# Performance work log

Hardware: AMD Instinct MI355X
Metric: run time of the kernel (lower is better)

## Reference

```python
import jax, jax.numpy as jnp
import numpy as np

N, E = 20000, 320000
FX, FW, FH, H = 256, 128, 128, 4  # x feat, walk feat, hidden=end_embd, heads


def _gat(x, edge_index, W, a_s, a_d, R):
    # W: [H,Fin,Fout]; a_s,a_d: [H,Fout]; R: [Fin,Fout] residual projection
    n = x.shape[0]
    h = jnp.einsum('nf,hfo->hno', x, W)                      # [H,N,Fout]
    src, dst = edge_index[0], edge_index[1]
    s_src = jnp.einsum('hno,ho->nh', h, a_s)                 # [N,H]
    s_dst = jnp.einsum('hno,ho->nh', h, a_d)                 # [N,H]
    e = jax.nn.leaky_relu(s_src[src] + s_dst[dst], 0.2)      # [E,H] per-edge scores
    m = jax.ops.segment_max(e, src, num_segments=n)          # scatter-softmax (stable)
    ex = jnp.exp(e - m[src])
    den = jax.ops.segment_sum(ex, src, num_segments=n)
    alpha = ex / (den[src] + 1e-16)                          # [E,H]
    msg = jnp.transpose(h, (1, 0, 2))[dst] * alpha[:, :, None]        # [E,H,Fout]
    agg = jax.ops.segment_sum(msg, src, num_segments=n).mean(axis=1)  # [N,Fout]
    return jax.nn.elu(agg + x @ R)


def _forward(x, dat, W1, a1s, a1d, R1, W2, a2s, a2d, R2,
             Wd1, ad1s, ad1d, Rd1, Wd2, ad2s, ad2d, Rd2,
             fc1_w, fc1_b, fc2_w, fc2_b, conv_w, conv_b, edge_index):
    x1 = _gat(x, edge_index, W1, a1s, a1d, R1)
    x2 = _gat(x1, edge_index, W2, a2s, a2d, R2)
    d1 = _gat(dat, edge_index, Wd1, ad1s, ad1d, Rd1)
    d2 = _gat(d1, edge_index, Wd2, ad2s, ad2d, Rd2)
    n = x.shape[0]
    # cat on feature dim, transpose, view(1, l*2, end_size, N)
    xd = jnp.concatenate([x1, x2, d1, d2], axis=1).T.reshape(1, 4, FH, n)
    avg = xd.mean(axis=(2, 3))                               # SE global avg pool [1,4]
    att = jax.nn.sigmoid((avg @ fc1_w + fc1_b) @ fc2_w + fc2_b)  # no act between fc1/fc2 (as in source)
    xatt = jax.nn.relu(att[:, :, None, None] * xd)
    y = jnp.einsum('bchn,c->bhn', xatt, conv_w) + conv_b     # 1x1 conv, 4->1 channels
    return y.reshape(FH, n).T                                # dropout = identity (eval)


def setup_inputs():
    key = jax.random.key(0)
    ks = jax.random.split(key, 26)

    def rn(k, shape, s=0.1):
        return jax.random.normal(k, shape, jnp.float32) * s

    return {
        'x': jax.random.normal(ks[0], (N, FX), jnp.float32),
        'dat': jax.random.normal(ks[1], (N, FW), jnp.float32),
        'W1': rn(ks[2], (H, FX, FH)), 'a1s': rn(ks[3], (H, FH)), 'a1d': rn(ks[4], (H, FH)), 'R1': rn(ks[5], (FX, FH)),
        'W2': rn(ks[6], (H, FH, FH)), 'a2s': rn(ks[7], (H, FH)), 'a2d': rn(ks[8], (H, FH)), 'R2': rn(ks[9], (FH, FH)),
        'Wd1': rn(ks[10], (H, FW, FH)), 'ad1s': rn(ks[11], (H, FH)), 'ad1d': rn(ks[12], (H, FH)), 'Rd1': rn(ks[13], (FW, FH)),
        'Wd2': rn(ks[14], (H, FH, FH)), 'ad2s': rn(ks[15], (H, FH)), 'ad2d': rn(ks[16], (H, FH)), 'Rd2': rn(ks[17], (FH, FH)),
        'fc1_w': rn(ks[18], (4, 20)), 'fc1_b': jnp.zeros((20,), jnp.float32),
        'fc2_w': rn(ks[19], (20, 4)), 'fc2_b': jnp.zeros((4,), jnp.float32),
        'conv_w': rn(ks[20], (4,)), 'conv_b': jnp.zeros((), jnp.float32),
        'edge_index': jax.random.randint(ks[21], (2, E), 0, N, dtype=jnp.int32),
    }


def reference(x, dat, W1, a1s, a1d, R1, W2, a2s, a2d, R2,
              Wd1, ad1s, ad1d, Rd1, Wd2, ad2s, ad2d, Rd2,
              fc1_w, fc1_b, fc2_w, fc2_b, conv_w, conv_b, edge_index):
    return _forward(x, dat, W1, a1s, a1d, R1, W2, a2s, a2d, R2,
                    Wd1, ad1s, ad1d, Rd1, Wd2, ad2s, ad2d, Rd2,
                    fc1_w, fc1_b, fc2_w, fc2_b, conv_w, conv_b, edge_index)
```

## Files before the change

### kernel.cpp

```cpp
#include <hip/hip_runtime.h>
#include <hip/hip_bf16.h>
#include <math.h>

#define NN 20000
#define EE 320000
#define FXX 256
#define FWW 128
#define NH 4

typedef __attribute__((ext_vector_type(8))) short short8v;
typedef __attribute__((ext_vector_type(4))) float f32x4;

static __device__ __forceinline__ float bf2f(unsigned short s) {
    unsigned int u = ((unsigned int)s) << 16;
    return __builtin_bit_cast(float, u);
}

static __device__ __forceinline__ unsigned short f2bf_u16(float f) {
    unsigned int u = __builtin_bit_cast(unsigned int, f);
    unsigned int r = 0x7fffu + ((u >> 16) & 1u);
    return (unsigned short)((u + r) >> 16);
}

struct WscItem { const float* W; const float* as_; const float* ad_; int Fin; };
struct WscParams { WscItem t[4]; };

__global__ __launch_bounds__(256) void wsc_kernel(WscParams p, float* __restrict__ wsc)
{
    int L = blockIdx.z;
    WscItem it = p.t[L];
    int wid = threadIdx.x >> 6, lane = threadIdx.x & 63;
    int r = blockIdx.x * 4 + wid;
    if (r >= it.Fin * 4) return;
    int h = r / it.Fin, k = r - h * it.Fin;
    float2 w2 = *(const float2*)(it.W + ((size_t)(h * it.Fin + k)) * 128 + 2 * lane);
    float2 s2 = *(const float2*)(it.as_ + h * 128 + 2 * lane);
    float2 d2 = *(const float2*)(it.ad_ + h * 128 + 2 * lane);
    float vs = w2.x * s2.x + w2.y * s2.y;
    float vd = w2.x * d2.x + w2.y * d2.y;
    #pragma unroll
    for (int o = 32; o; o >>= 1) { vs += __shfl_xor(vs, o); vd += __shfl_xor(vd, o); }
    if (lane == 0) {
        wsc[(size_t)L * 2048 + h * 256 + k] = vs;
        wsc[(size_t)L * 2048 + (4 + h) * 256 + k] = vd;
    }
}

struct WcItem { const float* W; const float* R; __hip_bfloat16* dst; int Fin; int KK; int total; };
struct WcParams { WcItem t[4]; };

__global__ __launch_bounds__(256) void wcomb_kernel(WcParams p)
{
    WcItem it = p.t[blockIdx.z];
    int idx = blockIdx.x * 256 + threadIdx.x;
    if (idx >= it.total) return;
    int c = idx / it.KK;
    int k5 = idx - c * it.KK;
    int f4 = it.Fin * 4;
    float v;
    if (k5 < f4) {
        int h = k5 / it.Fin, k = k5 - h * it.Fin;
        v = 0.25f * it.W[((size_t)(h * it.Fin + k)) * 128 + c];
    } else {
        v = it.R[(size_t)(k5 - f4) * 128 + c];
    }
    it.dst[(size_t)c * it.KK + k5] = __float2bfloat16(v);
}

template<int CF>
__global__ __launch_bounds__(256) void cast_score(const float* __restrict__ Xf,
                                                  __hip_bfloat16* __restrict__ Xb,
                                                  const float* __restrict__ wsc,
                                                  float* __restrict__ ssrc,
                                                  float* __restrict__ sdst)
{
    const int Fin = CF * 64;
    int wid = threadIdx.x >> 6, lane = threadIdx.x & 63;
    int n = blockIdx.x * 4 + wid;
    if (n >= NN) return;
    int c0 = lane * CF;
    float xv[CF];
    #pragma unroll
    for (int i = 0; i < CF; ++i) xv[i] = Xf[(size_t)n * Fin + c0 + i];
    union { unsigned u[CF / 2]; unsigned short s[CF]; } pk;
    #pragma unroll
    for (int i = 0; i < CF; ++i) pk.s[i] = f2bf_u16(xv[i]);
    #pragma unroll
    for (int w = 0; w < CF / 2; ++w)
        *(unsigned*)(Xb + (size_t)n * Fin + c0 + w * 2) = pk.u[w];
    float acc[8];
    #pragma unroll
    for (int j = 0; j < 8; ++j) {
        const float* w = wsc + j * 256 + c0;
        float s = 0.f;
        #pragma unroll
        for (int i = 0; i < CF; ++i) s += xv[i] * w[i];
        acc[j] = s;
    }
    #pragma unroll
    for (int o = 32; o; o >>= 1)
        #pragma unroll
        for (int j = 0; j < 8; ++j) acc[j] += __shfl_xor(acc[j], o);
    if (lane == 0) {
        *(float4*)(ssrc + (size_t)n * 4) = make_float4(acc[0], acc[1], acc[2], acc[3]);
        *(float4*)(sdst + (size_t)n * 4) = make_float4(acc[4], acc[5], acc[6], acc[7]);
    }
}

__global__ __launch_bounds__(256) void hist_kernel(const int* __restrict__ src, int* __restrict__ cnt)
{
    int i = blockIdx.x * blockDim.x + threadIdx.x;
    if (i < EE) atomicAdd(&cnt[src[i]], 1);
}

__global__ __launch_bounds__(1024) void scan_kernel(const int* __restrict__ cnt, int* __restrict__ row_ptr)
{
    __shared__ int lds[1024];
    int t = threadIdx.x;
    const int CH = 20;
    int start = t * CH, end = start + CH; if (end > NN) end = NN;
    int sum = 0;
    if (start < NN) for (int i = start; i < end; ++i) sum += cnt[i];
    lds[t] = sum;
    __syncthreads();
    for (int o = 1; o < 1024; o <<= 1) {
        int v = (t >= o) ? lds[t - o] : 0;
        __syncthreads();
        lds[t] += v;
        __syncthreads();
    }
    int run = lds[t] - sum;
    if (start < NN) for (int i = start; i < end; ++i) { row_ptr[i] = run; run += cnt[i]; }
    if (t == 1023) row_ptr[NN] = lds[1023];
}

__global__ __launch_bounds__(256) void scatter_kernel(const int* __restrict__ src,
                                                      const int* __restrict__ dst,
                                                      const int* __restrict__ row_ptr,
                                                      int* __restrict__ off,
                                                      int* __restrict__ csr_dst)
{
    int i = blockIdx.x * blockDim.x + threadIdx.x;
    if (i >= EE) return;
    int s = src[i];
    int p = row_ptr[s] + atomicAdd(&off[s], 1);
    csr_dst[p] = dst[i];
}

template<int CF>
__global__ __launch_bounds__(256) void agg_cat_kernel(const __hip_bfloat16* __restrict__ Xb,
                                                      const float* __restrict__ ssrc,
                                                      const float* __restrict__ sdst,
                                                      const int* __restrict__ row_ptr,
                                                      const int* __restrict__ csr_dst,
                                                      __hip_bfloat16* __restrict__ Cat)
{
    const int Fin = CF * 64, F4 = 4 * Fin;
    int wid = threadIdx.x >> 6, lane = threadIdx.x & 63;
    int n = blockIdx.x * 4 + wid;
    if (n >= NN) return;
    int r0 = row_ptr[n], r1 = row_ptr[n + 1];
    int deg = r1 - r0;

    float acc[4][CF] = {};

    if (deg > 0) {
        float4 sn = *(const float4*)(ssrc + (size_t)n * 4);
        auto comp_e = [&](int s, int& dout) -> float4 {
            int d = csr_dst[r0 + s];
            dout = d;
            float4 sd = *(const float4*)(sdst + (size_t)d * 4);
            float4 e; float v;
            v = sn.x + sd.x; e.x = v >= 0.f ? v : 0.2f * v;
            v = sn.y + sd.y; e.y = v >= 0.f ? v : 0.2f * v;
            v = sn.z + sd.z; e.z = v >= 0.f ? v : 0.2f * v;
            v = sn.w + sd.w; e.w = v >= 0.f ? v : 0.2f * v;
            return e;
        };

        float4 e0 = make_float4(-1e30f, -1e30f, -1e30f, -1e30f);
        int d0 = 0;
        if (lane < deg) e0 = comp_e(lane, d0);
        float4 m = e0;
        for (int s = lane + 64; s < deg; s += 64) {
            int dt; float4 ev = comp_e(s, dt);
            m.x = fmaxf(m.x, ev.x); m.y = fmaxf(m.y, ev.y);
            m.z = fmaxf(m.z, ev.z); m.w = fmaxf(m.w, ev.w);
        }
        #pragma unroll
        for (int o = 32; o; o >>= 1) {
            m.x = fmaxf(m.x, __shfl_xor(m.x, o));
            m.y = fmaxf(m.y, __shfl_xor(m.y, o));
            m.z = fmaxf(m.z, __shfl_xor(m.z, o));
            m.w = fmaxf(m.w, __shfl_xor(m.w, o));
        }
        float4 p0 = make_float4(0.f, 0.f, 0.f, 0.f);
        if (lane < deg) {
            p0.x = expf(e0.x - m.x); p0.y = expf(e0.y - m.y);
            p0.z = expf(e0.z - m.z); p0.w = expf(e0.w - m.w);
        }
        float4 den = p0;
        for (int s = lane + 64; s < deg; s += 64) {
            int dt; float4 ev = comp_e(s, dt);
            den.x += expf(ev.x - m.x); den.y += expf(ev.y - m.y);
            den.z += expf(ev.z - m.z); den.w += expf(ev.w - m.w);
        }
        #pragma unroll
        for (int o = 32; o; o >>= 1) {
            den.x += __shfl_xor(den.x, o); den.y += __shfl_xor(den.y, o);
            den.z += __shfl_xor(den.z, o); den.w += __shfl_xor(den.w, o);
        }
        den.x = 1.f / (den.x + 1e-16f); den.y = 1.f / (den.y + 1e-16f);
        den.z = 1.f / (den.z + 1e-16f); den.w = 1.f / (den.w + 1e-16f);

        float4 a0;
        a0.x = p0.x * den.x; a0.y = p0.y * den.y;
        a0.z = p0.z * den.z; a0.w = p0.w * den.w;

        int cnt0 = min(deg, 64);
        int last = cnt0 - 1;
        for (int base = 0; base < cnt0; base += 4) {
            int j1 = min(base + 1, last), j2 = min(base + 2, last), j3 = min(base + 3, last);
            int dv0 = __shfl(d0, base), dv1 = __shfl(d0, j1);
            int dv2 = __shfl(d0, j2),   dv3 = __shfl(d0, j3);
            union U { unsigned u[CF / 2]; unsigned short s[CF]; };
            U l0, l1, l2, l3;
            #pragma unroll
            for (int w = 0; w < CF / 2; ++w)
                l0.u[w] = *(const unsigned*)(Xb + (size_t)dv0 * Fin + lane * CF + w * 2);
            #pragma unroll
            for (int w = 0; w < CF / 2; ++w)
                l1.u[w] = *(const unsigned*)(Xb + (size_t)dv1 * Fin + lane * CF + w * 2);
            #pragma unroll
            for (int w = 0; w < CF / 2; ++w)
                l2.u[w] = *(const unsigned*)(Xb + (size_t)dv2 * Fin + lane * CF + w * 2);
            #pragma unroll
            for (int w = 0; w < CF / 2; ++w)
                l3.u[w] = *(const unsigned*)(Xb + (size_t)dv3 * Fin + lane * CF + w * 2);

            {
                float ax = __shfl(a0.x, base), ay = __shfl(a0.y, base);
                float az = __shfl(a0.z, base), aw = __shfl(a0.w, base);
                #pragma unroll
                for (int i = 0; i < CF; ++i) {
                    float xv = bf2f(l0.s[i]);
                    acc[0][i] += ax * xv; acc[1][i] += ay * xv;
                    acc[2][i] += az * xv; acc[3][i] += aw * xv;
                }
            }
            if (base + 1 < cnt0) {
                float ax = __shfl(a0.x, j1), ay = __shfl(a0.y, j1);
                float az = __shfl(a0.z, j1), aw = __shfl(a0.w, j1);
                #pragma unroll
                for (int i = 0; i < CF; ++i) {
                    float xv = bf2f(l1.s[i]);
                    acc[0][i] += ax * xv; acc[1][i] += ay * xv;
                    acc[2][i] += az * xv; acc[3][i] += aw * xv;
                }
            }
            if (base + 2 < cnt0) {
                float ax = __shfl(a0.x, j2), ay = __shfl(a0.y, j2);
                float az = __shfl(a0.z, j2), aw = __shfl(a0.w, j2);
                #pragma unroll
                for (int i = 0; i < CF; ++i) {
                    float xv = bf2f(l2.s[i]);
                    acc[0][i] += ax * xv; acc[1][i] += ay * xv;
                    acc[2][i] += az * xv; acc[3][i] += aw * xv;
                }
            }
            if (base + 3 < cnt0) {
                float ax = __shfl(a0.x, j3), ay = __shfl(a0.y, j3);
                float az = __shfl(a0.z, j3), aw = __shfl(a0.w, j3);
                #pragma unroll
                for (int i = 0; i < CF; ++i) {
                    float xv = bf2f(l3.s[i]);
                    acc[0][i] += ax * xv; acc[1][i] += ay * xv;
                    acc[2][i] += az * xv; acc[3][i] += aw * xv;
                }
            }
        }

        for (int r = r0 + 64; r < r1; r += 64) {
            int cnt = min(64, r1 - r);
            int d = 0;
            float4 a4 = make_float4(0.f, 0.f, 0.f, 0.f);
            if (r + lane < r1) {
                int dt;
                float4 ev = comp_e(r - r0 + lane, dt);
                d = dt;
                a4.x = expf(ev.x - m.x) * den.x; a4.y = expf(ev.y - m.y) * den.y;
                a4.z = expf(ev.z - m.z) * den.z; a4.w = expf(ev.w - m.w) * den.w;
            }
            for (int j = 0; j < cnt; ++j) {
                int ddv = __shfl(d, j);
                float ax = __shfl(a4.x, j), ay = __shfl(a4.y, j);
                float az = __shfl(a4.z, j), aw = __shfl(a4.w, j);
                union { unsigned u[CF / 2]; unsigned short s[CF]; } ld;
                #pragma unroll
                for (int w = 0; w < CF / 2; ++w)
                    ld.u[w] = *(const unsigned*)(Xb + (size_t)ddv * Fin + lane * CF + w * 2);
                #pragma unroll
                for (int i = 0; i < CF; ++i) {
                    float xv = bf2f(ld.s[i]);
                    acc[0][i] += ax * xv; acc[1][i] += ay * xv;
                    acc[2][i] += az * xv; acc[3][i] += aw * xv;
                }
            }
        }
    }

    __hip_bfloat16* crow = Cat + (size_t)n * F4;
    #pragma unroll
    for (int h = 0; h < 4; ++h) {
        union { unsigned u[CF / 2]; unsigned short s[CF]; } pk;
        #pragma unroll
        for (int i = 0; i < CF; ++i) pk.s[i] = f2bf_u16(acc[h][i]);
        #pragma unroll
        for (int w = 0; w < CF / 2; ++w)
            *(unsigned*)(crow + h * Fin + lane * CF + w * 2) = pk.u[w];
    }
}

template<int F4, int FIN, bool DOSC>
__global__ __launch_bounds__(256) void gemm_elu(const __hip_bfloat16* __restrict__ Cat,
                                                const __hip_bfloat16* __restrict__ Xb,
                                                const __hip_bfloat16* __restrict__ Wct,
                                                float* __restrict__ xout,
                                                __hip_bfloat16* __restrict__ xbout,
                                                float* __restrict__ sums, int ch,
                                                const float* __restrict__ wscN,
                                                float* __restrict__ ssrcN,
                                                float* __restrict__ sdstN)
{
    const int KK = F4 + FIN;
    const int BK = 64;
    const int NIT = KK / BK;
    __shared__ short As[2][32 * 72];
    __shared__ short Bs[2][128 * 72];
    __shared__ float ls[4];
    __shared__ float sred[4][4][4][8];

    int tid = threadIdx.x, lane = tid & 63, wid = tid >> 6;
    int wr = wid >> 1, wc = wid & 1;
    int ar = lane & 15, kg = lane >> 4;
    int row0 = blockIdx.x * 32;

    int a_row = tid >> 3, a_seg = tid & 7;
    int b_col = tid >> 1, b_seg0 = (tid & 1) * 4;

    const __hip_bfloat16* AgC = Cat + (size_t)(row0 + a_row) * F4 + a_seg * 8;
    const __hip_bfloat16* AgX = Xb + (size_t)(row0 + a_row) * FIN + a_seg * 8;
    const __hip_bfloat16* Bg = Wct + (size_t)b_col * KK + b_seg0 * 8;

    short8v fa, fb0, fb1, fb2, fb3;
    f32x4 acc[4] = {};

    fa  = *(const short8v*)(AgC);
    fb0 = *(const short8v*)(Bg);
    fb1 = *(const short8v*)(Bg + 8);
    fb2 = *(const short8v*)(Bg + 16);
    fb3 = *(const short8v*)(Bg + 24);
    *(short8v*)(&As[0][a_row * 72 + a_seg * 8]) = fa;
    *(short8v*)(&Bs[0][b_col * 72 + (b_seg0 + 0) * 8]) = fb0;
    *(short8v*)(&Bs[0][b_col * 72 + (b_seg0 + 1) * 8]) = fb1;
    *(short8v*)(&Bs[0][b_col * 72 + (b_seg0 + 2) * 8]) = fb2;
    *(short8v*)(&Bs[0][b_col * 72 + (b_seg0 + 3) * 8]) = fb3;

    int cur = 0;
    for (int it = 0; it < NIT; ++it) {
        if (it + 1 < NIT) {
            int kb = (it + 1) * BK;
            fa  = (kb < F4) ? *(const short8v*)(AgC + kb) : *(const short8v*)(AgX + (kb - F4));
            fb0 = *(const short8v*)(Bg + kb);
            fb1 = *(const short8v*)(Bg + kb + 8);
            fb2 = *(const short8v*)(Bg + kb + 16);
            fb3 = *(const short8v*)(Bg + kb + 24);
        }
        __syncthreads();
        #pragma unroll
        for (int ks = 0; ks < 2; ++ks) {
            short8v a = *(const short8v*)(&As[cur][(wr * 16 + ar) * 72 + ks * 32 + kg * 8]);
            #pragma unroll
            for (int nb = 0; nb < 4; ++nb) {
                short8v b = *(const short8v*)(&Bs[cur][(wc * 64 + nb * 16 + ar) * 72 + ks * 32 + kg * 8]);
                acc[nb] = __builtin_amdgcn_mfma_f32_16x16x32_bf16(a, b, acc[nb], 0, 0, 0);
            }
        }
        if (it + 1 < NIT) {
            int nb2 = cur ^ 1;
            *(short8v*)(&As[nb2][a_row * 72 + a_seg * 8]) = fa;
            *(short8v*)(&Bs[nb2][b_col * 72 + (b_seg0 + 0) * 8]) = fb0;
            *(short8v*)(&Bs[nb2][b_col * 72 + (b_seg0 + 1) * 8]) = fb1;
            *(short8v*)(&Bs[nb2][b_col * 72 + (b_seg0 + 2) * 8]) = fb2;
            *(short8v*)(&Bs[nb2][b_col * 72 + (b_seg0 + 3) * 8]) = fb3;
        }
        cur ^= 1;
    }

    float lsum = 0.f;
    float vpost[4][4];
    int rsub = (lane >> 4) * 4;
    #pragma unroll
    for (int nb = 0; nb < 4; ++nb) {
        int col = wc * 64 + nb * 16 + ar;
        #pragma unroll
        for (int r = 0; r < 4; ++r) {
            int row = row0 + wr * 16 + rsub + r;
            float v = acc[nb][r];
            v = v > 0.f ? v : expm1f(v);
            vpost[nb][r] = v;
            lsum += v;
            xout[(size_t)row * 128 + col] = v;
            xbout[(size_t)row * 128 + col] = __float2bfloat16(v);
        }
    }
    #pragma unroll
    for (int o = 32; o; o >>= 1) lsum += __shfl_xor(lsum, o);
    if (lane == 0) ls[wid] = lsum;

    if (DOSC) {
        float sc[4][8] = {};
        #pragma unroll
        for (int j = 0; j < 8; ++j) {
            #pragma unroll
            for (int nb = 0; nb < 4; ++nb) {
                float wv = wscN[j * 256 + wc * 64 + nb * 16 + ar];
                #pragma unroll
                for (int r = 0; r < 4; ++r) sc[r][j] += vpost[nb][r] * wv;
            }
        }
        #pragma unroll
        for (int o = 8; o; o >>= 1)
            #pragma unroll
            for (int r = 0; r < 4; ++r)
                #pragma unroll
                for (int j = 0; j < 8; ++j) sc[r][j] += __shfl_xor(sc[r][j], o);
        if (ar == 0) {
            int grp = lane >> 4;
            #pragma unroll
            for (int r = 0; r < 4; ++r)
                #pragma unroll
                for (int j = 0; j < 8; ++j) sred[wid][grp][r][j] = sc[r][j];
        }
    }
    __syncthreads();
    if (tid == 0) atomicAdd(&sums[ch], ls[0] + ls[1] + ls[2] + ls[3]);
    if (DOSC) {
        int row_local = tid >> 3, j = tid & 7;
        int w_r = row_local >> 4, grp = (row_local >> 2) & 3, r = row_local & 3;
        float total = sred[w_r * 2 + 0][grp][r][j] + sred[w_r * 2 + 1][grp][r][j];
        int row = row0 + row_local;
        if (j < 4) ssrcN[(size_t)row * 4 + j] = total;
        else       sdstN[(size_t)row * 4 + (j - 4)] = total;
    }
}

__global__ void att_kernel(const float* __restrict__ sums,
                           const float* __restrict__ fc1w, const float* __restrict__ fc1b,
                           const float* __restrict__ fc2w, const float* __restrict__ fc2b,
                           float* __restrict__ att)
{
    if (threadIdx.x != 0 || blockIdx.x != 0) return;
    float avg[4];
    for (int c = 0; c < 4; ++c) avg[c] = sums[c] * (1.f / (NN * 128.f));
    float z[20];
    for (int j = 0; j < 20; ++j) {
        float v = fc1b[j];
        for (int c = 0; c < 4; ++c) v += avg[c] * fc1w[c * 20 + j];
        z[j] = v;
    }
    for (int c = 0; c < 4; ++c) {
        float v = fc2b[c];
        for (int j = 0; j < 20; ++j) v += z[j] * fc2w[j * 4 + c];
        att[c] = 1.f / (1.f + expf(-v));
    }
}

__global__ __launch_bounds__(256) void final_kernel(const float* __restrict__ x1,
                                                    const float* __restrict__ x2,
                                                    const float* __restrict__ d1,
                                                    const float* __restrict__ d2,
                                                    const float* __restrict__ att,
                                                    const float* __restrict__ convw,
                                                    const float* __restrict__ convb,
                                                    float* __restrict__ out)
{
    int i = blockIdx.x * blockDim.x + threadIdx.x;
    if (i >= NN * 128) return;
    float a0 = att[0], a1 = att[1], a2 = att[2], a3 = att[3];
    float w0 = convw[0], w1 = convw[1], w2 = convw[2], w3 = convw[3];
    float v = convb[0];
    v += w0 * fmaxf(a0 * x1[i], 0.f);
    v += w1 * fmaxf(a1 * x2[i], 0.f);
    v += w2 * fmaxf(a2 * d1[i], 0.f);
    v += w3 * fmaxf(a3 * d2[i], 0.f);
    out[i] = v;
}

extern "C" void kernel_launch(void* const* d_in, const int* in_sizes, int n_in,
                              void* d_out, int out_size, void* d_ws, size_t ws_size,
                              hipStream_t stream)
{
    (void)in_sizes; (void)n_in; (void)out_size; (void)ws_size;
    const float* x    = (const float*)d_in[0];
    const float* dat  = (const float*)d_in[1];
    const float* W1   = (const float*)d_in[2];
    const float* a1s  = (const float*)d_in[3];
    const float* a1d  = (const float*)d_in[4];
    const float* R1   = (const float*)d_in[5];
    const float* W2   = (const float*)d_in[6];
    const float* a2s  = (const float*)d_in[7];
    const float* a2d  = (const float*)d_in[8];
    const float* R2   = (const float*)d_in[9];
    const float* Wd1  = (const float*)d_in[10];
    const float* ad1s = (const float*)d_in[11];
    const float* ad1d = (const float*)d_in[12];
    const float* Rd1  = (const float*)d_in[13];
    const float* Wd2  = (const float*)d_in[14];
    const float* ad2s = (const float*)d_in[15];
    const float* ad2d = (const float*)d_in[16];
    const float* Rd2  = (const float*)d_in[17];
    const float* fc1w = (const float*)d_in[18];
    const float* fc1b = (const float*)d_in[19];
    const float* fc2w = (const float*)d_in[20];
    const float* fc2b = (const float*)d_in[21];
    const float* convw= (const float*)d_in[22];
    const float* convb= (const float*)d_in[23];
    const int*   eidx = (const int*)d_in[24];
    const int* esrc = eidx;
    const int* edst = eidx + EE;
    float* out = (float*)d_out;

    char* base = (char*)d_ws;
    size_t woff = 0;
    auto alloc = [&](size_t bytes) -> void* {
        void* p = base + woff;
        woff = (woff + bytes + 255) & ~(size_t)255;
        return p;
    };
    __hip_bfloat16* Cat  = (__hip_bfloat16*)alloc((size_t)NN * 1024 * 2);
    float* X1    = (float*)alloc((size_t)NN * 128 * 4);
    float* X2    = (float*)alloc((size_t)NN * 128 * 4);
    float* D1    = (float*)alloc((size_t)NN * 128 * 4);
    float* D2    = (float*)alloc((size_t)NN * 128 * 4);
    __hip_bfloat16* XbX   = (__hip_bfloat16*)alloc((size_t)NN * FXX * 2);
    __hip_bfloat16* XbDat = (__hip_bfloat16*)alloc((size_t)NN * FWW * 2);
    __hip_bfloat16* Xb1   = (__hip_bfloat16*)alloc((size_t)NN * 128 * 2);
    __hip_bfloat16* XbD1  = (__hip_bfloat16*)alloc((size_t)NN * 128 * 2);
    __hip_bfloat16* XbTmp = (__hip_bfloat16*)alloc((size_t)NN * 128 * 2);
    float* Wsc   = (float*)alloc((size_t)4 * 2048 * 4);
    __hip_bfloat16* Wct0 = (__hip_bfloat16*)alloc((size_t)128 * 1280 * 2);
    __hip_bfloat16* Wct1 = (__hip_bfloat16*)alloc((size_t)128 * 640 * 2);
    __hip_bfloat16* Wct2 = (__hip_bfloat16*)alloc((size_t)128 * 640 * 2);
    __hip_bfloat16* Wct3 = (__hip_bfloat16*)alloc((size_t)128 * 640 * 2);
    float* SsrcX = (float*)alloc((size_t)NN * 4 * 4);
    float* SdstX = (float*)alloc((size_t)NN * 4 * 4);
    float* Ssrc1 = (float*)alloc((size_t)NN * 4 * 4);
    float* Sdst1 = (float*)alloc((size_t)NN * 4 * 4);
    float* SsrcD = (float*)alloc((size_t)NN * 4 * 4);
    float* SdstD = (float*)alloc((size_t)NN * 4 * 4);
    float* Ssrc3 = (float*)alloc((size_t)NN * 4 * 4);
    float* Sdst3 = (float*)alloc((size_t)NN * 4 * 4);
    int* RowPtr  = (int*)alloc((size_t)(NN + 1) * 4);
    int* Cnt     = (int*)alloc((size_t)NN * 4);
    int* Off     = (int*)alloc((size_t)NN * 4);
    int* CsrDst  = (int*)alloc((size_t)EE * 4);
    float* Sums  = (float*)alloc(16);
    float* Att   = (float*)alloc(16);

    {
        WscParams WP;
        WP.t[0] = { W1,  a1s,  a1d,  FXX };
        WP.t[1] = { W2,  a2s,  a2d,  FWW };
        WP.t[2] = { Wd1, ad1s, ad1d, FWW };
        WP.t[3] = { Wd2, ad2s, ad2d, FWW };
        wsc_kernel<<<dim3(256, 1, 4), 256, 0, stream>>>(WP, Wsc);
        WcParams CP;
        CP.t[0] = { W1,  R1,  Wct0, FXX, 1280, 128 * 1280 };
        CP.t[1] = { W2,  R2,  Wct1, FWW, 640,  128 * 640 };
        CP.t[2] = { Wd1, Rd1, Wct2, FWW, 640,  128 * 640 };
        CP.t[3] = { Wd2, Rd2, Wct3, FWW, 640,  128 * 640 };
        wcomb_kernel<<<dim3(640, 1, 4), 256, 0, stream>>>(CP);
        cast_score<4><<<(NN + 3) / 4, 256, 0, stream>>>(x, XbX, Wsc, SsrcX, SdstX);
        cast_score<2><<<(NN + 3) / 4, 256, 0, stream>>>(dat, XbDat, Wsc + 2 * 2048, SsrcD, SdstD);
    }
    hipMemsetAsync(Cnt, 0, (size_t)NN * 4, stream);
    hipMemsetAsync(Off, 0, (size_t)NN * 4, stream);
    hipMemsetAsync(Sums, 0, 16, stream);
    hist_kernel<<<(EE + 255) / 256, 256, 0, stream>>>(esrc, Cnt);
    scan_kernel<<<1, 1024, 0, stream>>>(Cnt, RowPtr);
    scatter_kernel<<<(EE + 255) / 256, 256, 0, stream>>>(esrc, edst, RowPtr, Off, CsrDst);

    agg_cat_kernel<4><<<(NN + 3) / 4, 256, 0, stream>>>(XbX, SsrcX, SdstX, RowPtr, CsrDst, Cat);
    gemm_elu<1024, 256, true><<<NN / 32, 256, 0, stream>>>(Cat, XbX, Wct0, X1, Xb1, Sums, 0,
                                                           Wsc + 1 * 2048, Ssrc1, Sdst1);
    agg_cat_kernel<2><<<(NN + 3) / 4, 256, 0, stream>>>(Xb1, Ssrc1, Sdst1, RowPtr, CsrDst, Cat);
    gemm_elu<512, 128, false><<<NN / 32, 256, 0, stream>>>(Cat, Xb1, Wct1, X2, XbTmp, Sums, 1,
                                                           nullptr, nullptr, nullptr);
    agg_cat_kernel<2><<<(NN + 3) / 4, 256, 0, stream>>>(XbDat, SsrcD, SdstD, RowPtr, CsrDst, Cat);
    gemm_elu<512, 128, true><<<NN / 32, 256, 0, stream>>>(Cat, XbDat, Wct2, D1, XbD1, Sums, 2,
                                                          Wsc + 3 * 2048, Ssrc3, Sdst3);
    agg_cat_kernel<2><<<(NN + 3) / 4, 256, 0, stream>>>(XbD1, Ssrc3, Sdst3, RowPtr, CsrDst, Cat);
    gemm_elu<512, 128, false><<<NN / 32, 256, 0, stream>>>(Cat, XbD1, Wct3, D2, XbTmp, Sums, 3,
                                                           nullptr, nullptr, nullptr);

    att_kernel<<<1, 64, 0, stream>>>(Sums, fc1w, fc1b, fc2w, fc2b, Att);
    final_kernel<<<(NN * 128 + 255) / 256, 256, 0, stream>>>(X1, X2, D1, D2, Att, convw, convb, out);
}
```

Before: 339.5 us.

## Batch independent x and dat GAT branches into paired kernel launches

The x-branch and dat-branch GAT layers are independent, so their cast/score, aggregation and GEMM stages are now launched together with blockIdx.y selecting the branch. This halves the number of sequential launches and doubles the grid per launch, aiming to fill the GPU better and cut launch and tail overhead. The cost is a separate Cat buffer for each branch, and the GEMM's template parameters F4/FIN/DOSC become runtime values, which may lose compile-time unrolling and constant folding in the GEMM inner loop.

Measured after the change: 307.4 us. 9.5% less time.

```diff
diff --git a/kernel.cpp b/kernel.cpp
--- a/kernel.cpp
+++ b/kernel.cpp
@@ -68,11 +68,11 @@
 }
 
 template<int CF>
-__global__ __launch_bounds__(256) void cast_score(const float* __restrict__ Xf,
-                                                  __hip_bfloat16* __restrict__ Xb,
-                                                  const float* __restrict__ wsc,
-                                                  float* __restrict__ ssrc,
-                                                  float* __restrict__ sdst)
+static __device__ __forceinline__ void cast_score_body(const float* __restrict__ Xf,
+                                                       __hip_bfloat16* __restrict__ Xb,
+                                                       const float* __restrict__ wsc,
+                                                       float* __restrict__ ssrc,
+                                                       float* __restrict__ sdst)
 {
     const int Fin = CF * 64;
     int wid = threadIdx.x >> 6, lane = threadIdx.x & 63;
@@ -105,6 +105,19 @@
         *(float4*)(ssrc + (size_t)n * 4) = make_float4(acc[0], acc[1], acc[2], acc[3]);
         *(float4*)(sdst + (size_t)n * 4) = make_float4(acc[4], acc[5], acc[6], acc[7]);
     }
+}
+
+struct CSPair {
+    const float* Xf[2]; __hip_bfloat16* Xb[2];
+    const float* wsc[2]; float* ssrc[2]; float* sdst[2];
+};
+
+__global__ __launch_bounds__(256) void cast_score_pair(CSPair p)
+{
+    if (blockIdx.y == 0)
+        cast_score_body<4>(p.Xf[0], p.Xb[0], p.wsc[0], p.ssrc[0], p.sdst[0]);
+    else
+        cast_score_body<2>(p.Xf[1], p.Xb[1], p.wsc[1], p.ssrc[1], p.sdst[1]);
 }
 
 __global__ __launch_bounds__(256) void hist_kernel(const int* __restrict__ src, int* __restrict__ cnt)
@@ -148,12 +161,12 @@
 }
 
 template<int CF>
-__global__ __launch_bounds__(256) void agg_cat_kernel(const __hip_bfloat16* __restrict__ Xb,
-                                                      const float* __restrict__ ssrc,
-                                                      const float* __restrict__ sdst,
-                                                      const int* __restrict__ row_ptr,
-                                                      const int* __restrict__ csr_dst,
-                                                      __hip_bfloat16* __restrict__ Cat)
+static __device__ __forceinline__ void agg_body(const __hip_bfloat16* __restrict__ Xb,
+                                                const float* __restrict__ ssrc,
+                                                const float* __restrict__ sdst,
+                                                const int* __restrict__ row_ptr,
+                                                const int* __restrict__ csr_dst,
+                                                __hip_bfloat16* __restrict__ Cat)
 {
     const int Fin = CF * 64, F4 = 4 * Fin;
     int wid = threadIdx.x >> 6, lane = threadIdx.x & 63;
@@ -321,17 +334,35 @@
     }
 }
 
-template<int F4, int FIN, bool DOSC>
-__global__ __launch_bounds__(256) void gemm_elu(const __hip_bfloat16* __restrict__ Cat,
-                                                const __hip_bfloat16* __restrict__ Xb,
-                                                const __hip_bfloat16* __restrict__ Wct,
-                                                float* __restrict__ xout,
-                                                __hip_bfloat16* __restrict__ xbout,
-                                                float* __restrict__ sums, int ch,
-                                                const float* __restrict__ wscN,
-                                                float* __restrict__ ssrcN,
-                                                float* __restrict__ sdstN)
-{
+struct AggPair {
+    const __hip_bfloat16* Xb[2];
+    const float* ssrc[2]; const float* sdst[2];
+    __hip_bfloat16* Cat[2];
+};
+
+template<int CF0, int CF1>
+__global__ __launch_bounds__(256) void agg_pair_kernel(AggPair p,
+                                                       const int* __restrict__ row_ptr,
+                                                       const int* __restrict__ csr_dst)
+{
+    if (blockIdx.y == 0)
+        agg_body<CF0>(p.Xb[0], p.ssrc[0], p.sdst[0], row_ptr, csr_dst, p.Cat[0]);
+    else
+        agg_body<CF1>(p.Xb[1], p.ssrc[1], p.sdst[1], row_ptr, csr_dst, p.Cat[1]);
+}
+
+struct GemmArgs {
+    const __hip_bfloat16 *Cat, *Xb, *Wct;
+    float* xout; __hip_bfloat16* xbout;
+    const float* wscN; float *ssrcN, *sdstN;
+    int F4, FIN, ch;
+};
+struct GemmPair { GemmArgs g[2]; };
+
+__global__ __launch_bounds__(256) void gemm_pair_kernel(GemmPair p, float* __restrict__ sums)
+{
+    GemmArgs a = (blockIdx.y == 0) ? p.g[0] : p.g[1];
+    const int F4 = a.F4, FIN = a.FIN;
     const int KK = F4 + FIN;
     const int BK = 64;
     const int NIT = KK / BK;
@@ -348,9 +379,9 @@
     int a_row = tid >> 3, a_seg = tid & 7;
     int b_col = tid >> 1, b_seg0 = (tid & 1) * 4;
 
-    const __hip_bfloat16* AgC = Cat + (size_t)(row0 + a_row) * F4 + a_seg * 8;
-    const __hip_bfloat16* AgX = Xb + (size_t)(row0 + a_row) * FIN + a_seg * 8;
-    const __hip_bfloat16* Bg = Wct + (size_t)b_col * KK + b_seg0 * 8;
+    const __hip_bfloat16* AgC = a.Cat + (size_t)(row0 + a_row) * F4 + a_seg * 8;
+    const __hip_bfloat16* AgX = a.Xb + (size_t)(row0 + a_row) * FIN + a_seg * 8;
+    const __hip_bfloat16* Bg = a.Wct + (size_t)b_col * KK + b_seg0 * 8;
 
     short8v fa, fb0, fb1, fb2, fb3;
     f32x4 acc[4] = {};
@@ -379,11 +410,11 @@
         __syncthreads();
         #pragma unroll
         for (int ks = 0; ks < 2; ++ks) {
-            short8v a = *(const short8v*)(&As[cur][(wr * 16 + ar) * 72 + ks * 32 + kg * 8]);
+            short8v av = *(const short8v*)(&As[cur][(wr * 16 + ar) * 72 + ks * 32 + kg * 8]);
             #pragma unroll
             for (int nb = 0; nb < 4; ++nb) {
-                short8v b = *(const short8v*)(&Bs[cur][(wc * 64 + nb * 16 + ar) * 72 + ks * 32 + kg * 8]);
-                acc[nb] = __builtin_amdgcn_mfma_f32_16x16x32_bf16(a, b, acc[nb], 0, 0, 0);
+                short8v bv = *(const short8v*)(&Bs[cur][(wc * 64 + nb * 16 + ar) * 72 + ks * 32 + kg * 8]);
+                acc[nb] = __builtin_amdgcn_mfma_f32_16x16x32_bf16(av, bv, acc[nb], 0, 0, 0);
             }
         }
         if (it + 1 < NIT) {
@@ -410,21 +441,22 @@
             v = v > 0.f ? v : expm1f(v);
             vpost[nb][r] = v;
             lsum += v;
-            xout[(size_t)row * 128 + col] = v;
-            xbout[(size_t)row * 128 + col] = __float2bfloat16(v);
+            a.xout[(size_t)row * 128 + col] = v;
+            a.xbout[(size_t)row * 128 + col] = __float2bfloat16(v);
         }
     }
     #pragma unroll
     for (int o = 32; o; o >>= 1) lsum += __shfl_xor(lsum, o);
     if (lane == 0) ls[wid] = lsum;
 
-    if (DOSC) {
+    bool dosc = a.wscN != nullptr;
+    if (dosc) {
         float sc[4][8] = {};
         #pragma unroll
         for (int j = 0; j < 8; ++j) {
             #pragma unroll
             for (int nb = 0; nb < 4; ++nb) {
-                float wv = wscN[j * 256 + wc * 64 + nb * 16 + ar];
+                float wv = a.wscN[j * 256 + wc * 64 + nb * 16 + ar];
                 #pragma unroll
                 for (int r = 0; r < 4; ++r) sc[r][j] += vpost[nb][r] * wv;
             }
@@ -444,14 +476,14 @@
         }
     }
     __syncthreads();
-    if (tid == 0) atomicAdd(&sums[ch], ls[0] + ls[1] + ls[2] + ls[3]);
-    if (DOSC) {
+    if (tid == 0) atomicAdd(&sums[a.ch], ls[0] + ls[1] + ls[2] + ls[3]);
+    if (dosc) {
         int row_local = tid >> 3, j = tid & 7;
         int w_r = row_local >> 4, grp = (row_local >> 2) & 3, r = row_local & 3;
         float total = sred[w_r * 2 + 0][grp][r][j] + sred[w_r * 2 + 1][grp][r][j];
         int row = row0 + row_local;
-        if (j < 4) ssrcN[(size_t)row * 4 + j] = total;
-        else       sdstN[(size_t)row * 4 + (j - 4)] = total;
+        if (j < 4) a.ssrcN[(size_t)row * 4 + j] = total;
+        else       a.sdstN[(size_t)row * 4 + (j - 4)] = total;
     }
 }
 
@@ -538,7 +570,8 @@
         woff = (woff + bytes + 255) & ~(size_t)255;
         return p;
     };
-    __hip_bfloat16* Cat  = (__hip_bfloat16*)alloc((size_t)NN * 1024 * 2);
+    __hip_bfloat16* Cat0 = (__hip_bfloat16*)alloc((size_t)NN * 1024 * 2);
+    __hip_bfloat16* Cat2 = (__hip_bfloat16*)alloc((size_t)NN * 512 * 2);
     float* X1    = (float*)alloc((size_t)NN * 128 * 4);
     float* X2    = (float*)alloc((size_t)NN * 128 * 4);
     float* D1    = (float*)alloc((size_t)NN * 128 * 4);
@@ -548,6 +581,7 @@
     __hip_bfloat16* Xb1   = (__hip_bfloat16*)alloc((size_t)NN * 128 * 2);
     __hip_bfloat16* XbD1  = (__hip_bfloat16*)alloc((size_t)NN * 128 * 2);
     __hip_bfloat16* XbTmp = (__hip_bfloat16*)alloc((size_t)NN * 128 * 2);
+    __hip_bfloat16* XbTm2 = (__hip_bfloat16*)alloc((size_t)NN * 128 * 2);
     float* Wsc   = (float*)alloc((size_t)4 * 2048 * 4);
     __hip_bfloat16* Wct0 = (__hip_bfloat16*)alloc((size_t)128 * 1280 * 2);
     __hip_bfloat16* Wct1 = (__hip_bfloat16*)alloc((size_t)128 * 640 * 2);
@@ -581,8 +615,10 @@
         CP.t[2] = { Wd1, Rd1, Wct2, FWW, 640,  128 * 640 };
         CP.t[3] = { Wd2, Rd2, Wct3, FWW, 640,  128 * 640 };
         wcomb_kernel<<<dim3(640, 1, 4), 256, 0, stream>>>(CP);
-        cast_score<4><<<(NN + 3) / 4, 256, 0, stream>>>(x, XbX, Wsc, SsrcX, SdstX);
-        cast_score<2><<<(NN + 3) / 4, 256, 0, stream>>>(dat, XbDat, Wsc + 2 * 2048, SsrcD, SdstD);
+        CSPair CS;
+        CS.Xf[0] = x;   CS.Xb[0] = XbX;   CS.wsc[0] = Wsc;            CS.ssrc[0] = SsrcX; CS.sdst[0] = SdstX;
+        CS.Xf[1] = dat; CS.Xb[1] = XbDat; CS.wsc[1] = Wsc + 2 * 2048; CS.ssrc[1] = SsrcD; CS.sdst[1] = SdstD;
+        cast_score_pair<<<dim3((NN + 3) / 4, 2), 256, 0, stream>>>(CS);
     }
     hipMemsetAsync(Cnt, 0, (size_t)NN * 4, stream);
     hipMemsetAsync(Off, 0, (size_t)NN * 4, stream);
@@ -591,18 +627,30 @@
     scan_kernel<<<1, 1024, 0, stream>>>(Cnt, RowPtr);
     scatter_kernel<<<(EE + 255) / 256, 256, 0, stream>>>(esrc, edst, RowPtr, Off, CsrDst);
 
-    agg_cat_kernel<4><<<(NN + 3) / 4, 256, 0, stream>>>(XbX, SsrcX, SdstX, RowPtr, CsrDst, Cat);
-    gemm_elu<1024, 256, true><<<NN / 32, 256, 0, stream>>>(Cat, XbX, Wct0, X1, Xb1, Sums, 0,
-                                                           Wsc + 1 * 2048, Ssrc1, Sdst1);
-    agg_cat_kernel<2><<<(NN + 3) / 4, 256, 0, stream>>>(Xb1, Ssrc1, Sdst1, RowPtr, CsrDst, Cat);
-    gemm_elu<512, 128, false><<<NN / 32, 256, 0, stream>>>(Cat, Xb1, Wct1, X2, XbTmp, Sums, 1,
-                                                           nullptr, nullptr, nullptr);
-    agg_cat_kernel<2><<<(NN + 3) / 4, 256, 0, stream>>>(XbDat, SsrcD, SdstD, RowPtr, CsrDst, Cat);
-    gemm_elu<512, 128, true><<<NN / 32, 256, 0, stream>>>(Cat, XbDat, Wct2, D1, XbD1, Sums, 2,
-                                                          Wsc + 3 * 2048, Ssrc3, Sdst3);
-    agg_cat_kernel<2><<<(NN + 3) / 4, 256, 0, stream>>>(XbD1, Ssrc3, Sdst3, RowPtr, CsrDst, Cat);
-    gemm_elu<512, 128, false><<<NN / 32, 256, 0, stream>>>(Cat, XbD1, Wct3, D2, XbTmp, Sums, 3,
-                                                           nullptr, nullptr, nullptr);
+    {
+        AggPair AP;
+        AP.Xb[0] = XbX;   AP.ssrc[0] = SsrcX; AP.sdst[0] = SdstX; AP.Cat[0] = Cat0;
+        AP.Xb[1] = XbDat; AP.ssrc[1] = SsrcD; AP.sdst[1] = SdstD; AP.Cat[1] = Cat2;
+        agg_pair_kernel<4, 2><<<dim3((NN + 3) / 4, 2), 256, 0, stream>>>(AP, RowPtr, CsrDst);
+    }
+    {
+        GemmPair GP;
+        GP.g[0] = { Cat0, XbX,   Wct0, X1, Xb1,  Wsc + 1 * 2048, Ssrc1, Sdst1, 1024, 256, 0 };
+        GP.g[1] = { Cat2, XbDat, Wct2, D1, XbD1, Wsc + 3 * 2048, Ssrc3, Sdst3, 512,  128, 2 };
+        gemm_pair_kernel<<<dim3(NN / 32, 2), 256, 0, stream>>>(GP, Sums);
+    }
+    {
+        AggPair AP;
+        AP.Xb[0] = Xb1;  AP.ssrc[0] = Ssrc1; AP.sdst[0] = Sdst1; AP.Cat[0] = Cat0;
+        AP.Xb[1] = XbD1; AP.ssrc[1] = Ssrc3; AP.sdst[1] = Sdst3; AP.Cat[1] = Cat2;
+        agg_pair_kernel<2, 2><<<dim3((NN + 3) / 4, 2), 256, 0, stream>>>(AP, RowPtr, CsrDst);
+    }
+    {
+        GemmPair GP;
+        GP.g[0] = { Cat0, Xb1,  Wct1, X2, XbTmp, nullptr, nullptr, nullptr, 512, 128, 1 };
+        GP.g[1] = { Cat2, XbD1, Wct3, D2, XbTm2, nullptr, nullptr, nullptr, 512, 128, 3 };
+        gemm_pair_kernel<<<dim3(NN / 32, 2), 256, 0, stream>>>(GP, Sums);
+    }
 
     att_kernel<<<1, 64, 0, stream>>>(Sums, fc1w, fc1b, fc2w, fc2b, Att);
     final_kernel<<<(NN * 128 + 255) / 256, 256, 0, stream>>>(X1, X2, D1, D2, Att, convw, convb, out);
```
